# Optimization experiments

Measured on AMD Instinct MI355X. Metric: run time of the kernel, lower is better.

## Reference

```python
import jax, jax.numpy as jnp
import numpy as np
import math

N_KEYS = 2048      # set size (number of pragma keys)
EMB = 768          # embed_size
KEY_E = 512        # key_embed_size
VAL_E = 256        # val_embed_size (KEY_E + VAL_E == EMB)
CAT_VOCAB = 100000 # categorical embedding rows
N_REG = 1000       # integer-key embedding rows / per-key Linear(1,256) encoders
HID = 512          # hidden_size (dim_V)
HEADS = 8
N_OUT = 7          # PMA num_outputs
SCALE = math.sqrt(HID)  # original divides by sqrt(dim_V), not sqrt(head_dim)


def _split_heads(x):
    # torch: torch.cat(x.split(dim_V//h, 2), 0)  -> [h*B, N, dim_V/h]
    return jnp.concatenate(jnp.split(x, HEADS, axis=2), axis=0)


def _merge_heads(x):
    # torch: torch.cat(x.split(B, 0), 2)
    return jnp.concatenate(jnp.split(x, HEADS, axis=0), axis=2)


def _mab(Q, K, wq, bq, wk, bk, wv, bv, wo, bo):
    # MAB with ln=False: project, head-split along batch, attend, residual, relu FF residual
    Qp = Q @ wq.T + bq
    Kp = K @ wk.T + bk
    Vp = K @ wv.T + bv
    Q_, K_, V_ = _split_heads(Qp), _split_heads(Kp), _split_heads(Vp)
    A = jax.nn.softmax(jnp.einsum('bqd,bkd->bqk', Q_, K_) / SCALE, axis=-1)
    O = _merge_heads(Q_ + jnp.einsum('bqk,bkd->bqd', A, V_))
    return O + jax.nn.relu(O @ wo.T + bo)


def _forward(reg_values, cat_table, reg_table, reg_W, reg_b,
             q0_w, q0_b, k0_w, k0_b, v0_w, v0_b, o0_w, o0_b,
             qs_w, qs_b, ks_w, ks_b, vs_w, vs_b, os_w, os_b,
             S, pq_w, pq_b, pk_w, pk_b, pv_w, pv_b, po_w, po_b,
             fc_w, fc_b, is_cat, cat_idx, reg_idx):
    # vectorized form of the per-key python loop: gather -> tiny linear encode -> select
    val_emb = reg_W[reg_idx] * reg_values[:, None] + reg_b[reg_idx]     # [N, VAL_E]
    reg_full = jnp.concatenate([reg_table[reg_idx], val_emb], axis=-1)  # [N, EMB]
    emb = jnp.where(is_cat[:, None], cat_table[cat_idx], reg_full)[None]  # [1, N, EMB]
    x = _mab(emb, emb, q0_w, q0_b, k0_w, k0_b, v0_w, v0_b, o0_w, o0_b)
    for i in range(3):
        x = _mab(x, x, qs_w[i], qs_b[i], ks_w[i], ks_b[i], vs_w[i], vs_b[i], os_w[i], os_b[i])
    # decoder: PMA (MAB(S, X)) then Linear(HID, 1)
    s = jnp.broadcast_to(S, (x.shape[0], N_OUT, HID))
    p = _mab(s, x, pq_w, pq_b, pk_w, pk_b, pv_w, pv_b, po_w, po_b)      # [1, N_OUT, HID]
    return (p @ fc_w.T + fc_b).reshape(-1)                              # [N_OUT]


def setup_inputs() -> dict:
    key = jax.random.key(0)
    ks = iter(jax.random.split(key, 48))
    def w(shape, s=0.02):
        return jax.random.normal(next(ks), shape, jnp.float32) * s
    inp = {}
    inp['is_cat'] = jax.random.bernoulli(next(ks), 0.5, (N_KEYS,))
    inp['cat_idx'] = jax.random.randint(next(ks), (N_KEYS,), 0, CAT_VOCAB)
    inp['reg_idx'] = jax.random.randint(next(ks), (N_KEYS,), 0, N_REG)
    inp['reg_values'] = jax.random.uniform(next(ks), (N_KEYS,), jnp.float32, 1.0, 64.0)
    inp['cat_table'] = w((CAT_VOCAB, EMB), 0.05)
    inp['reg_table'] = w((N_REG, KEY_E), 0.05)
    inp['reg_W'] = w((N_REG, VAL_E))
    inp['reg_b'] = w((N_REG, VAL_E))
    inp['q0_w'] = w((HID, EMB)); inp['q0_b'] = w((HID,))
    inp['k0_w'] = w((HID, EMB)); inp['k0_b'] = w((HID,))
    inp['v0_w'] = w((HID, EMB)); inp['v0_b'] = w((HID,))
    inp['o0_w'] = w((HID, HID)); inp['o0_b'] = w((HID,))
    for nm in ['qs', 'ks', 'vs', 'os']:
        inp[nm + '_w'] = w((3, HID, HID))
        inp[nm + '_b'] = w((3, HID))
    inp['S'] = w((1, N_OUT, HID), 0.05)
    for nm in ['pq', 'pk', 'pv', 'po']:
        inp[nm + '_w'] = w((HID, HID))
        inp[nm + '_b'] = w((HID,))
    inp['fc_w'] = w((1, HID)); inp['fc_b'] = w((1,))
    return inp


def reference(is_cat, cat_idx, reg_idx, reg_values, cat_table, reg_table, reg_W, reg_b,
              q0_w, q0_b, k0_w, k0_b, v0_w, v0_b, o0_w, o0_b,
              qs_w, qs_b, ks_w, ks_b, vs_w, vs_b, os_w, os_b,
              S, pq_w, pq_b, pk_w, pk_b, pv_w, pv_b, po_w, po_b, fc_w, fc_b):
    return _forward(reg_values, cat_table, reg_table, reg_W, reg_b,
                    q0_w, q0_b, k0_w, k0_b, v0_w, v0_b, o0_w, o0_b,
                    qs_w, qs_b, ks_w, ks_b, vs_w, vs_b, os_w, os_b,
                    S, pq_w, pq_b, pk_w, pk_b, pv_w, pv_b, po_w, po_b,
                    fc_w, fc_b, is_cat, cat_idx, reg_idx)
```

## Files before the change

### kernel.cpp

```cpp
#include <hip/hip_runtime.h>
#include <stdint.h>


#define HID 512
#define EMBD 768
#define NCTX 2048
#define HD 64

typedef __attribute__((ext_vector_type(8))) short v8s;
typedef __attribute__((ext_vector_type(4))) float v4f;

#define MFMA(a, b, c) __builtin_amdgcn_mfma_f32_16x16x32_bf16((a), (b), (c), 0, 0, 0)

__device__ __forceinline__ short f2bf(float f) {
  uint32_t u = __builtin_bit_cast(uint32_t, f);
  uint32_t r = (u + 0x7FFFu + ((u >> 16) & 1u)) >> 16;
  return (short)r;
}
__device__ __forceinline__ float bf2f(short s) {
  uint32_t u = ((uint32_t)(uint16_t)s) << 16;
  return __builtin_bit_cast(float, u);
}
__device__ __forceinline__ v8s ldbf8(const short* p) { return *(const v8s*)p; }

struct ConvDesc {
  const float* src[20];
  unsigned cum[21];
};

__global__ void k_convert(ConvDesc d, short* __restrict__ dst) {
  unsigned i = blockIdx.x * 256u + threadIdx.x;
  if (i >= d.cum[20]) return;
  int t = 0;
  while (i >= d.cum[t + 1]) ++t;
  dst[i] = f2bf(d.src[t][i - d.cum[t]]);
}

__global__ void k_emb(const int* __restrict__ is_cat, const int* __restrict__ cat_idx,
                      const int* __restrict__ reg_idx, const float* __restrict__ reg_values,
                      const float* __restrict__ cat_table, const float* __restrict__ reg_table,
                      const float* __restrict__ reg_W, const float* __restrict__ reg_b,
                      short* __restrict__ out) {
  int i = blockIdx.x * 256 + threadIdx.x;
  int n = i / EMBD, e = i - n * EMBD;
  float v;
  if (is_cat[n]) {
    v = cat_table[(long)cat_idx[n] * EMBD + e];
  } else {
    int r = reg_idx[n];
    if (e < 512) v = reg_table[r * 512 + e];
    else {
      int e2 = e - 512;
      v = reg_W[r * 256 + e2] * reg_values[n] + reg_b[r * 256 + e2];
    }
  }
  out[i] = f2bf(v);
}

__global__ void k_sbuild(const float* __restrict__ S, short* __restrict__ out) {
  int i = blockIdx.x * 256 + threadIdx.x;
  int row = i >> 9;
  out[i] = (row < 7) ? f2bf(S[i]) : (short)0;
}

template <int EPI, int KK>
__global__ __launch_bounds__(64) void k_gemm(const short* __restrict__ A,
                                             const short* __restrict__ B,
                                             const float* __restrict__ biasA,
                                             const float* __restrict__ biasB,
                                             const short* __restrict__ resid,
                                             short* __restrict__ out, int N) {
  int l = threadIdx.x, l16 = l & 15, quad = l >> 4;
  int i0 = blockIdx.y * 32, n0 = blockIdx.x * 64;
  const short* a0p = A + (i0 + l16) * KK + quad * 8;
  const short* a1p = a0p + 16 * KK;
  const short* bp = B + (n0 + l16) * KK + quad * 8;
  v4f acc[2][4];
  for (int g = 0; g < 2; ++g)
    for (int t = 0; t < 4; ++t) acc[g][t] = (v4f){0.f, 0.f, 0.f, 0.f};
#pragma unroll 4
  for (int k = 0; k < KK; k += 32) {
    v8s a0 = ldbf8(a0p + k);
    v8s a1 = ldbf8(a1p + k);
#pragma unroll
    for (int t = 0; t < 4; ++t) {
      v8s b = ldbf8(bp + t * 16 * KK + k);
      acc[0][t] = MFMA(a0, b, acc[0][t]);
      acc[1][t] = MFMA(a1, b, acc[1][t]);
    }
  }
  for (int g = 0; g < 2; ++g)
    for (int t = 0; t < 4; ++t) {
      int col = n0 + t * 16 + l16;
      float bc;
      if (EPI == 0) bc = (col < 512) ? biasA[col] : biasB[col - 512];
      else if (EPI == 2) bc = biasA[col];
      else bc = 0.f;
      for (int r = 0; r < 4; ++r) {
        int row = i0 + g * 16 + quad * 4 + r;
        float v = acc[g][t][r];
        if (EPI == 0) v += bc;
        else if (EPI == 1) v += biasA[row];
        else v = bf2f(resid[row * N + col]) + fmaxf(v + bc, 0.f);
        out[row * N + col] = f2bf(v);
      }
    }
}

__global__ __launch_bounds__(256) void k_flash(const short* __restrict__ Q, int qstride,
                                               const short* __restrict__ Kp, int kstride,
                                               const short* __restrict__ Vt,
                                               float* __restrict__ opart,
                                               float* __restrict__ lspart) {
  __shared__ __align__(16) short Kt[64 * 64];
  __shared__ __align__(16) short Vtl[64 * 64];
  __shared__ __align__(16) short P[4][16 * 72];
  const int tid = threadIdx.x;
  const int wave = tid >> 6, l = tid & 63, l16 = l & 15, quad = l >> 4;
  const int h = blockIdx.y, D0 = h * HD;
  const int i0 = blockIdx.x * 64 + wave * 16;
  const int z = blockIdx.z, jbase = z * (NCTX / 4);

  const short* qrow = Q + (i0 + l16) * qstride + D0 + quad * 8;
  const v8s aq0 = ldbf8(qrow);
  const v8s aq1 = ldbf8(qrow + 32);

  const int sr = tid >> 2, sc0 = tid & 3, sc1 = sc0 + 4;
  const short* kg = Kp + (jbase + sr) * kstride + D0;
  const short* vg = Vt + (D0 + sr) * NCTX + jbase;
  short* kl0 = &Kt[(sr * 8 + (sc0 ^ (sr & 7))) * 8];
  short* kl1 = &Kt[(sr * 8 + (sc1 ^ (sr & 7))) * 8];
  short* vl0 = &Vtl[(sr * 8 + (sc0 ^ (sr & 7))) * 8];
  short* vl1 = &Vtl[(sr * 8 + (sc1 ^ (sr & 7))) * 8];

  v4f o[4];
  float lsum[4];
  for (int t = 0; t < 4; ++t) o[t] = (v4f){0.f, 0.f, 0.f, 0.f};
  for (int r = 0; r < 4; ++r) lsum[r] = 0.f;

  v8s pk0 = ldbf8(kg + sc0 * 8), pk1 = ldbf8(kg + sc1 * 8);
  v8s pv0 = ldbf8(vg + sc0 * 8), pv1 = ldbf8(vg + sc1 * 8);

  const float C2 = 0.06375872f;

  for (int j0 = 0; j0 < NCTX / 4; j0 += 64) {
    __syncthreads();
    *(v8s*)kl0 = pk0; *(v8s*)kl1 = pk1;
    *(v8s*)vl0 = pv0; *(v8s*)vl1 = pv1;
    __syncthreads();
    int jn = j0 + 64;
    if (jn < NCTX / 4) {
      pk0 = ldbf8(kg + jn * kstride + sc0 * 8);
      pk1 = ldbf8(kg + jn * kstride + sc1 * 8);
      pv0 = ldbf8(vg + jn + sc0 * 8);
      pv1 = ldbf8(vg + jn + sc1 * 8);
    }
    v4f s[4];
#pragma unroll
    for (int kt = 0; kt < 4; ++kt) {
      int R = kt * 16 + l16;
      v8s kb0 = *(const v8s*)&Kt[(R * 8 + (quad ^ (R & 7))) * 8];
      v8s kb1 = *(const v8s*)&Kt[(R * 8 + ((quad + 4) ^ (R & 7))) * 8];
      v4f t0 = (v4f){0.f, 0.f, 0.f, 0.f};
      t0 = MFMA(aq0, kb0, t0);
      s[kt] = MFMA(aq1, kb1, t0);
    }
    short* pw = &P[wave][0];
#pragma unroll
    for (int kt = 0; kt < 4; ++kt)
      for (int r = 0; r < 4; ++r) {
        float p = exp2f(fminf(s[kt][r] * C2, 40.f));
        lsum[r] += p;
        pw[(quad * 4 + r) * 72 + kt * 16 + l16] = f2bf(p);
      }
    asm volatile("s_waitcnt lgkmcnt(0)" ::: "memory");
    v8s pa0 = *(const v8s*)&pw[l16 * 72 + quad * 8];
    v8s pa1 = *(const v8s*)&pw[l16 * 72 + 32 + quad * 8];
#pragma unroll
    for (int t = 0; t < 4; ++t) {
      int R = t * 16 + l16;
      v8s bv0 = *(const v8s*)&Vtl[(R * 8 + (quad ^ (R & 7))) * 8];
      v8s bv1 = *(const v8s*)&Vtl[(R * 8 + ((quad + 4) ^ (R & 7))) * 8];
      o[t] = MFMA(pa0, bv0, o[t]);
      o[t] = MFMA(pa1, bv1, o[t]);
    }
  }
  for (int r = 0; r < 4; ++r) {
    lsum[r] += __shfl_xor(lsum[r], 1);
    lsum[r] += __shfl_xor(lsum[r], 2);
    lsum[r] += __shfl_xor(lsum[r], 4);
    lsum[r] += __shfl_xor(lsum[r], 8);
  }
  float* ob = opart + (size_t)z * (NCTX * HID);
  for (int t = 0; t < 4; ++t)
    for (int r = 0; r < 4; ++r)
      ob[(i0 + quad * 4 + r) * HID + D0 + t * 16 + l16] = o[t][r];
  if (l16 == 0)
    for (int r = 0; r < 4; ++r)
      lspart[z * (8 * NCTX) + h * NCTX + i0 + quad * 4 + r] = lsum[r];
}

__global__ void k_combine(const float* __restrict__ op, const float* __restrict__ ls,
                          const short* __restrict__ Qr, int qstride,
                          short* __restrict__ out) {
  const int PS = NCTX * HID;
  int i = blockIdx.x * 256 + threadIdx.x;
  int row = i >> 9, col = i & 511, h = col >> 6;
  float o = op[i] + op[i + PS] + op[i + 2 * PS] + op[i + 3 * PS];
  int li = h * NCTX + row;
  float d = ls[li] + ls[li + 8 * NCTX] + ls[li + 16 * NCTX] + ls[li + 24 * NCTX];
  out[i] = f2bf(bf2f(Qr[row * qstride + col]) + o / d);
}

__global__ __launch_bounds__(64) void k_fc(const short* __restrict__ P,
                                           const float* __restrict__ fcw,
                                           const float* __restrict__ fcb,
                                           float* __restrict__ out) {
  int j = blockIdx.x, l = threadIdx.x;
  float s = 0.f;
  int d0 = l * 8;
  for (int d = d0; d < d0 + 8; ++d) s += bf2f(P[j * HID + d]) * fcw[d];
  for (int msk = 1; msk < 64; msk <<= 1) s += __shfl_xor(s, msk);
  if (l == 0) out[j] = s + fcb[0];
}

extern "C" void kernel_launch(void* const* d_in, const int* in_sizes, int n_in,
                              void* d_out, int out_size, void* d_ws, size_t ws_size,
                              hipStream_t stream) {
  const int* is_cat = (const int*)d_in[0];
  const int* cat_idx = (const int*)d_in[1];
  const int* reg_idx = (const int*)d_in[2];
  const float* reg_values = (const float*)d_in[3];
  const float* cat_table = (const float*)d_in[4];
  const float* reg_table = (const float*)d_in[5];
  const float* reg_W = (const float*)d_in[6];
  const float* reg_b = (const float*)d_in[7];
  const float* q0_w = (const float*)d_in[8];  const float* q0_b = (const float*)d_in[9];
  const float* k0_w = (const float*)d_in[10]; const float* k0_b = (const float*)d_in[11];
  const float* v0_w = (const float*)d_in[12]; const float* v0_b = (const float*)d_in[13];
  const float* o0_w = (const float*)d_in[14]; const float* o0_b = (const float*)d_in[15];
  const float* qs_w = (const float*)d_in[16]; const float* qs_b = (const float*)d_in[17];
  const float* ks_w = (const float*)d_in[18]; const float* ks_b = (const float*)d_in[19];
  const float* vs_w = (const float*)d_in[20]; const float* vs_b = (const float*)d_in[21];
  const float* os_w = (const float*)d_in[22]; const float* os_b = (const float*)d_in[23];
  const float* S    = (const float*)d_in[24];
  const float* pq_w = (const float*)d_in[25]; const float* pq_b = (const float*)d_in[26];
  const float* pk_w = (const float*)d_in[27]; const float* pk_b = (const float*)d_in[28];
  const float* pv_w = (const float*)d_in[29]; const float* pv_b = (const float*)d_in[30];
  const float* po_w = (const float*)d_in[31]; const float* po_b = (const float*)d_in[32];
  const float* fc_w = (const float*)d_in[33]; const float* fc_b = (const float*)d_in[34];

  short* W = (short*)d_ws;

  const unsigned OWQK[4] = {0u, 1441792u, 2490368u, 3538944u};
  const unsigned OWV[4]  = {786432u, 1966080u, 3014656u, 4063232u};
  const unsigned OWO[4]  = {1179648u, 2228224u, 3276800u, 4325376u};
  const unsigned OPQW = 4587520u, OPKW = 4849664u, OPVW = 5111808u, OPOW = 5373952u;
  const unsigned TOTW = 5636096u;
  const unsigned OEMB = TOTW;
  const unsigned OXA  = OEMB + 1572864u;
  const unsigned OXB  = OXA + 1048576u;
  const unsigned OQK  = OXB + 1048576u;
  const unsigned OVT  = OQK + 2097152u;
  const unsigned OOH  = OVT + 1048576u;
  const unsigned OSB  = OOH + 1048576u;
  const unsigned OQPP = OSB + 32768u;
  const unsigned OKPP = OQPP + 32768u;
  const unsigned OOHP = OKPP + 1048576u;
  const unsigned OPP  = OOHP + 32768u;
  const unsigned OF32 = OPP + 32768u;
  float* F = (float*)(W + OF32);
  float* LS = F + 4u * 1048576u;

  ConvDesc cd;
  const float* srcs[20] = {
      q0_w, k0_w, v0_w, o0_w,
      qs_w, ks_w, vs_w, os_w,
      qs_w + 262144, ks_w + 262144, vs_w + 262144, os_w + 262144,
      qs_w + 524288, ks_w + 524288, vs_w + 524288, os_w + 524288,
      pq_w, pk_w, pv_w, po_w};
  const unsigned cums[21] = {0u,       393216u,  786432u,  1179648u, 1441792u,
                             1703936u, 1966080u, 2228224u, 2490368u, 2752512u,
                             3014656u, 3276800u, 3538944u, 3801088u, 4063232u,
                             4325376u, 4587520u, 4849664u, 5111808u, 5373952u,
                             5636096u};
  for (int i = 0; i < 20; ++i) cd.src[i] = srcs[i];
  for (int i = 0; i < 21; ++i) cd.cum[i] = cums[i];
  k_convert<<<(TOTW + 255) / 256, 256, 0, stream>>>(cd, W);

  k_emb<<<(2048 * 768) / 256, 256, 0, stream>>>(is_cat, cat_idx, reg_idx, reg_values,
                                                cat_table, reg_table, reg_W, reg_b,
                                                W + OEMB);
  k_sbuild<<<(64 * 512) / 256, 256, 0, stream>>>(S, W + OSB);

  const float* bq[4] = {q0_b, qs_b, qs_b + 512, qs_b + 1024};
  const float* bk[4] = {k0_b, ks_b, ks_b + 512, ks_b + 1024};
  const float* bv[4] = {v0_b, vs_b, vs_b + 512, vs_b + 1024};
  const float* bo[4] = {o0_b, os_b, os_b + 512, os_b + 1024};
  const unsigned oxin[4]  = {OEMB, OXA, OXB, OXA};
  const unsigned oxout[4] = {OXA, OXB, OXA, OXB};

  dim3 gqk(16, 64);
  dim3 gv(32, 16);
  dim3 go(8, 64);
  dim3 gf(32, 8, 4);

  for (int l = 0; l < 4; ++l) {
    const short* X = W + oxin[l];
    short* Xout = W + oxout[l];
    if (l == 0) {
      k_gemm<0, 768><<<gqk, 64, 0, stream>>>(X, W + OWQK[0], bq[0], bk[0], nullptr, W + OQK, 1024);
      k_gemm<1, 768><<<gv, 64, 0, stream>>>(W + OWV[0], X, bv[0], bv[0], nullptr, W + OVT, 2048);
    } else {
      k_gemm<0, 512><<<gqk, 64, 0, stream>>>(X, W + OWQK[l], bq[l], bk[l], nullptr, W + OQK, 1024);
      k_gemm<1, 512><<<gv, 64, 0, stream>>>(W + OWV[l], X, bv[l], bv[l], nullptr, W + OVT, 2048);
    }
    k_flash<<<gf, 256, 0, stream>>>(W + OQK, 1024, W + OQK + 512, 1024, W + OVT, F, LS);
    k_combine<<<(2048 * 512) / 256, 256, 0, stream>>>(F, LS, W + OQK, 1024, W + OOH);
    k_gemm<2, 512><<<go, 64, 0, stream>>>(W + OOH, W + OWO[l], bo[l], bo[l], W + OOH, Xout, 512);
  }

  k_gemm<0, 512><<<dim3(8, 2), 64, 0, stream>>>(W + OSB, W + OPQW, pq_b, pq_b, nullptr, W + OQPP, 512);
  k_gemm<0, 512><<<dim3(8, 64), 64, 0, stream>>>(W + OXB, W + OPKW, pk_b, pk_b, nullptr, W + OKPP, 512);
  k_gemm<1, 512><<<dim3(32, 16), 64, 0, stream>>>(W + OPVW, W + OXB, pv_b, pv_b, nullptr, W + OVT, 2048);
  k_flash<<<dim3(1, 8, 4), 256, 0, stream>>>(W + OQPP, 512, W + OKPP, 512, W + OVT, F, LS);
  k_combine<<<(16 * 512) / 256, 256, 0, stream>>>(F, LS, W + OQPP, 512, W + OOHP);
  k_gemm<2, 512><<<dim3(8, 1), 64, 0, stream>>>(W + OOHP, W + OPOW, po_b, po_b, W + OOHP, W + OPP, 512);
  k_fc<<<7, 64, 0, stream>>>(W + OPP, fc_w, fc_b, (float*)d_out);
}
```

Baseline: 739.7 us.

## Merge prep kernels and batch independent GEMMs into multi-job launches

Folds weight conversion, embedding gathering and S construction into one prep kernel, and merges the QK and V projection GEMMs (and the three PMA projection GEMMs) into a single launch that dispatches jobs by block index. The softmax scale constant moves out of the flash inner loop into the K-projection epilogue, removing a multiply per score. bf16 conversion now uses the library intrinsic. This cuts launch count and gives each launch more blocks to fill the GPU, at the cost of runtime-indexed job descriptors and KK, which are no longer compile-time constants and so limit unrolling.

```diff
diff --git a/kernel.cpp b/kernel.cpp
--- a/kernel.cpp
+++ b/kernel.cpp
@@ -1,4 +1,5 @@
 #include <hip/hip_runtime.h>
+#include <hip/hip_bf16.h>
 #include <stdint.h>
 
 
@@ -13,9 +14,7 @@
 #define MFMA(a, b, c) __builtin_amdgcn_mfma_f32_16x16x32_bf16((a), (b), (c), 0, 0, 0)
 
 __device__ __forceinline__ short f2bf(float f) {
-  uint32_t u = __builtin_bit_cast(uint32_t, f);
-  uint32_t r = (u + 0x7FFFu + ((u >> 16) & 1u)) >> 16;
-  return (short)r;
+  return __builtin_bit_cast(short, __float2bfloat16(f));
 }
 __device__ __forceinline__ float bf2f(short s) {
   uint32_t u = ((uint32_t)(uint16_t)s) << 16;
@@ -28,48 +27,112 @@
   unsigned cum[21];
 };
 
-__global__ void k_convert(ConvDesc d, short* __restrict__ dst) {
-  unsigned i = blockIdx.x * 256u + threadIdx.x;
-  if (i >= d.cum[20]) return;
-  int t = 0;
-  while (i >= d.cum[t + 1]) ++t;
-  dst[i] = f2bf(d.src[t][i - d.cum[t]]);
-}
-
-__global__ void k_emb(const int* __restrict__ is_cat, const int* __restrict__ cat_idx,
-                      const int* __restrict__ reg_idx, const float* __restrict__ reg_values,
-                      const float* __restrict__ cat_table, const float* __restrict__ reg_table,
-                      const float* __restrict__ reg_W, const float* __restrict__ reg_b,
-                      short* __restrict__ out) {
-  int i = blockIdx.x * 256 + threadIdx.x;
-  int n = i / EMBD, e = i - n * EMBD;
-  float v;
-  if (is_cat[n]) {
-    v = cat_table[(long)cat_idx[n] * EMBD + e];
+#define NB_CONV 22016u
+#define NB_EMB 6144u
+#define NB_S 128u
+
+__global__ __launch_bounds__(256) void k_prep(
+    ConvDesc d, short* __restrict__ Wdst,
+    const int* __restrict__ is_cat, const int* __restrict__ cat_idx,
+    const int* __restrict__ reg_idx, const float* __restrict__ reg_values,
+    const float* __restrict__ cat_table, const float* __restrict__ reg_table,
+    const float* __restrict__ reg_W, const float* __restrict__ reg_b,
+    short* __restrict__ emb_out, const float* __restrict__ S,
+    short* __restrict__ s_out) {
+  unsigned b = blockIdx.x;
+  if (b < NB_CONV) {
+    unsigned i = b * 256u + threadIdx.x;
+    if (i >= d.cum[20]) return;
+    int t = 0;
+    while (i >= d.cum[t + 1]) ++t;
+    Wdst[i] = f2bf(d.src[t][i - d.cum[t]]);
+  } else if (b < NB_CONV + NB_EMB) {
+    int i = (int)(b - NB_CONV) * 256 + threadIdx.x;
+    int n = i / EMBD, e = i - n * EMBD;
+    float v;
+    if (is_cat[n]) {
+      v = cat_table[(long)cat_idx[n] * EMBD + e];
+    } else {
+      int r = reg_idx[n];
+      if (e < 512) v = reg_table[r * 512 + e];
+      else {
+        int e2 = e - 512;
+        v = reg_W[r * 256 + e2] * reg_values[n] + reg_b[r * 256 + e2];
+      }
+    }
+    emb_out[i] = f2bf(v);
   } else {
-    int r = reg_idx[n];
-    if (e < 512) v = reg_table[r * 512 + e];
-    else {
-      int e2 = e - 512;
-      v = reg_W[r * 256 + e2] * reg_values[n] + reg_b[r * 256 + e2];
-    }
-  }
-  out[i] = f2bf(v);
-}
-
-__global__ void k_sbuild(const float* __restrict__ S, short* __restrict__ out) {
-  int i = blockIdx.x * 256 + threadIdx.x;
-  int row = i >> 9;
-  out[i] = (row < 7) ? f2bf(S[i]) : (short)0;
-}
-
-template <int EPI, int KK>
-__global__ __launch_bounds__(64) void k_gemm(const short* __restrict__ A,
-                                             const short* __restrict__ B,
-                                             const float* __restrict__ biasA,
-                                             const float* __restrict__ biasB,
-                                             const short* __restrict__ resid,
-                                             short* __restrict__ out, int N) {
+    int i = (int)(b - NB_CONV - NB_EMB) * 256 + threadIdx.x;
+    int row = i >> 9;
+    s_out[i] = (row < 7) ? f2bf(S[i]) : (short)0;
+  }
+}
+
+struct GemmJob {
+  const short* A;
+  const short* B;
+  const float* biasA;
+  const float* biasB;
+  short* out;
+  int N, KK, epi, gx, base;
+  float sA, sB;
+};
+struct GemmBatch {
+  GemmJob j[3];
+  int nj;
+};
+
+__global__ __launch_bounds__(64) void k_gemm_multi(GemmBatch gb) {
+  int wg = blockIdx.x;
+  int ji = 0;
+  if (gb.nj > 1 && wg >= gb.j[1].base) ji = 1;
+  if (gb.nj > 2 && wg >= gb.j[2].base) ji = 2;
+  const GemmJob& j = gb.j[ji];
+  int rel = wg - j.base;
+  int bx = rel % j.gx, by = rel / j.gx;
+  int l = threadIdx.x, l16 = l & 15, quad = l >> 4;
+  int i0 = by * 32, n0 = bx * 64;
+  const int KK = j.KK;
+  const short* a0p = j.A + (i0 + l16) * KK + quad * 8;
+  const short* a1p = a0p + 16 * KK;
+  const short* bp = j.B + (n0 + l16) * KK + quad * 8;
+  v4f acc[2][4];
+  for (int g = 0; g < 2; ++g)
+    for (int t = 0; t < 4; ++t) acc[g][t] = (v4f){0.f, 0.f, 0.f, 0.f};
+#pragma unroll 4
+  for (int k = 0; k < KK; k += 32) {
+    v8s a0 = ldbf8(a0p + k);
+    v8s a1 = ldbf8(a1p + k);
+#pragma unroll
+    for (int t = 0; t < 4; ++t) {
+      v8s b = ldbf8(bp + t * 16 * KK + k);
+      acc[0][t] = MFMA(a0, b, acc[0][t]);
+      acc[1][t] = MFMA(a1, b, acc[1][t]);
+    }
+  }
+  for (int g = 0; g < 2; ++g)
+    for (int t = 0; t < 4; ++t) {
+      int col = n0 + t * 16 + l16;
+      float bc = 0.f, sc = 1.f;
+      if (j.epi == 0) {
+        bc = (col < 512) ? j.biasA[col] : j.biasB[col - 512];
+        sc = (col < 512) ? j.sA : j.sB;
+      }
+      for (int r = 0; r < 4; ++r) {
+        int row = i0 + g * 16 + quad * 4 + r;
+        float v = acc[g][t][r];
+        v = (j.epi == 0) ? (v + bc) * sc : v + j.biasA[row];
+        j.out[row * j.N + col] = f2bf(v);
+      }
+    }
+}
+
+template <int KK>
+__global__ __launch_bounds__(64) void k_gemm_ff(const short* __restrict__ A,
+                                               const short* __restrict__ B,
+                                               const float* __restrict__ biasA,
+                                               const short* __restrict__ resid,
+                                               short* __restrict__ out, int N) {
   int l = threadIdx.x, l16 = l & 15, quad = l >> 4;
   int i0 = blockIdx.y * 32, n0 = blockIdx.x * 64;
   const short* a0p = A + (i0 + l16) * KK + quad * 8;
@@ -92,16 +155,10 @@
   for (int g = 0; g < 2; ++g)
     for (int t = 0; t < 4; ++t) {
       int col = n0 + t * 16 + l16;
-      float bc;
-      if (EPI == 0) bc = (col < 512) ? biasA[col] : biasB[col - 512];
-      else if (EPI == 2) bc = biasA[col];
-      else bc = 0.f;
+      float bc = biasA[col];
       for (int r = 0; r < 4; ++r) {
         int row = i0 + g * 16 + quad * 4 + r;
-        float v = acc[g][t][r];
-        if (EPI == 0) v += bc;
-        else if (EPI == 1) v += biasA[row];
-        else v = bf2f(resid[row * N + col]) + fmaxf(v + bc, 0.f);
+        float v = bf2f(resid[row * N + col]) + fmaxf(acc[g][t][r] + bc, 0.f);
         out[row * N + col] = f2bf(v);
       }
     }
@@ -141,8 +198,6 @@
   v8s pk0 = ldbf8(kg + sc0 * 8), pk1 = ldbf8(kg + sc1 * 8);
   v8s pv0 = ldbf8(vg + sc0 * 8), pv1 = ldbf8(vg + sc1 * 8);
 
-  const float C2 = 0.06375872f;
-
   for (int j0 = 0; j0 < NCTX / 4; j0 += 64) {
     __syncthreads();
     *(v8s*)kl0 = pk0; *(v8s*)kl1 = pk1;
@@ -169,7 +224,7 @@
 #pragma unroll
     for (int kt = 0; kt < 4; ++kt)
       for (int r = 0; r < 4; ++r) {
-        float p = exp2f(fminf(s[kt][r] * C2, 40.f));
+        float p = exp2f(fminf(s[kt][r], 40.f));
         lsum[r] += p;
         pw[(quad * 4 + r) * 72 + kt * 16 + l16] = f2bf(p);
       }
@@ -272,6 +327,8 @@
   float* F = (float*)(W + OF32);
   float* LS = F + 4u * 1048576u;
 
+  const float C2 = 0.06375872f;
+
   ConvDesc cd;
   const float* srcs[20] = {
       q0_w, k0_w, v0_w, o0_w,
@@ -286,12 +343,9 @@
                              5636096u};
   for (int i = 0; i < 20; ++i) cd.src[i] = srcs[i];
   for (int i = 0; i < 21; ++i) cd.cum[i] = cums[i];
-  k_convert<<<(TOTW + 255) / 256, 256, 0, stream>>>(cd, W);
-
-  k_emb<<<(2048 * 768) / 256, 256, 0, stream>>>(is_cat, cat_idx, reg_idx, reg_values,
-                                                cat_table, reg_table, reg_W, reg_b,
-                                                W + OEMB);
-  k_sbuild<<<(64 * 512) / 256, 256, 0, stream>>>(S, W + OSB);
+  k_prep<<<NB_CONV + NB_EMB + NB_S, 256, 0, stream>>>(
+      cd, W, is_cat, cat_idx, reg_idx, reg_values, cat_table, reg_table,
+      reg_W, reg_b, W + OEMB, S, W + OSB);
 
   const float* bq[4] = {q0_b, qs_b, qs_b + 512, qs_b + 1024};
   const float* bk[4] = {k0_b, ks_b, ks_b + 512, ks_b + 1024};
@@ -300,31 +354,30 @@
   const unsigned oxin[4]  = {OEMB, OXA, OXB, OXA};
   const unsigned oxout[4] = {OXA, OXB, OXA, OXB};
 
-  dim3 gqk(16, 64);
-  dim3 gv(32, 16);
-  dim3 go(8, 64);
   dim3 gf(32, 8, 4);
 
   for (int l = 0; l < 4; ++l) {
     const short* X = W + oxin[l];
     short* Xout = W + oxout[l];
-    if (l == 0) {
-      k_gemm<0, 768><<<gqk, 64, 0, stream>>>(X, W + OWQK[0], bq[0], bk[0], nullptr, W + OQK, 1024);
-      k_gemm<1, 768><<<gv, 64, 0, stream>>>(W + OWV[0], X, bv[0], bv[0], nullptr, W + OVT, 2048);
-    } else {
-      k_gemm<0, 512><<<gqk, 64, 0, stream>>>(X, W + OWQK[l], bq[l], bk[l], nullptr, W + OQK, 1024);
-      k_gemm<1, 512><<<gv, 64, 0, stream>>>(W + OWV[l], X, bv[l], bv[l], nullptr, W + OVT, 2048);
-    }
+    int KKl = (l == 0) ? 768 : 512;
+    GemmBatch gb{};
+    gb.nj = 2;
+    gb.j[0] = {X, W + OWQK[l], bq[l], bk[l], W + OQK, 1024, KKl, 0, 16, 0, 1.f, C2};
+    gb.j[1] = {W + OWV[l], X, bv[l], nullptr, W + OVT, 2048, KKl, 1, 32, 1024, 1.f, 1.f};
+    k_gemm_multi<<<1536, 64, 0, stream>>>(gb);
     k_flash<<<gf, 256, 0, stream>>>(W + OQK, 1024, W + OQK + 512, 1024, W + OVT, F, LS);
     k_combine<<<(2048 * 512) / 256, 256, 0, stream>>>(F, LS, W + OQK, 1024, W + OOH);
-    k_gemm<2, 512><<<go, 64, 0, stream>>>(W + OOH, W + OWO[l], bo[l], bo[l], W + OOH, Xout, 512);
-  }
-
-  k_gemm<0, 512><<<dim3(8, 2), 64, 0, stream>>>(W + OSB, W + OPQW, pq_b, pq_b, nullptr, W + OQPP, 512);
-  k_gemm<0, 512><<<dim3(8, 64), 64, 0, stream>>>(W + OXB, W + OPKW, pk_b, pk_b, nullptr, W + OKPP, 512);
-  k_gemm<1, 512><<<dim3(32, 16), 64, 0, stream>>>(W + OPVW, W + OXB, pv_b, pv_b, nullptr, W + OVT, 2048);
+    k_gemm_ff<512><<<dim3(8, 64), 64, 0, stream>>>(W + OOH, W + OWO[l], bo[l], W + OOH, Xout, 512);
+  }
+
+  GemmBatch gp{};
+  gp.nj = 3;
+  gp.j[0] = {W + OSB, W + OPQW, pq_b, pq_b, W + OQPP, 512, 512, 0, 8, 0, 1.f, 1.f};
+  gp.j[1] = {W + OXB, W + OPKW, pk_b, pk_b, W + OKPP, 512, 512, 0, 8, 16, C2, C2};
+  gp.j[2] = {W + OPVW, W + OXB, pv_b, nullptr, W + OVT, 2048, 512, 1, 32, 528, 1.f, 1.f};
+  k_gemm_multi<<<1040, 64, 0, stream>>>(gp);
   k_flash<<<dim3(1, 8, 4), 256, 0, stream>>>(W + OQPP, 512, W + OKPP, 512, W + OVT, F, LS);
   k_combine<<<(16 * 512) / 256, 256, 0, stream>>>(F, LS, W + OQPP, 512, W + OOHP);
-  k_gemm<2, 512><<<dim3(8, 1), 64, 0, stream>>>(W + OOHP, W + OPOW, po_b, po_b, W + OOHP, W + OPP, 512);
+  k_gemm_ff<512><<<dim3(8, 1), 64, 0, stream>>>(W + OOHP, W + OPOW, po_b, W + OOHP, W + OPP, 512);
   k_fc<<<7, 64, 0, stream>>>(W + OPP, fc_w, fc_b, (float*)d_out);
 }
```

Result: no change. 728.0 us (-1.6%).
